# Kernel optimization log

Measured on AMD Instinct MI355X. Metric: run time of the kernel, lower is better.

## Reference

```python
import jax, jax.numpy as jnp
import numpy as np

B = 4096        # batch_size
D = 256         # feature_dim
N = 9000000     # dataset size (state buffer length)
G = 100         # num_groups
ALPHA = 0.5     # alpha_weight
GAMMA = 0.8
RHO = 8.0
LAM = 1.0       # lambada
ETA_P = 0.01
EPS = 1e-14
CLIP = 5.0


def setup_inputs() -> dict:
    key = jax.random.key(0)
    k = jax.random.split(key, 6)
    zis = jax.random.normal(k[0], (B, D), jnp.float32)
    zjs = jax.random.normal(k[1], (B, D), jnp.float32)
    # per-sample learned temperatures, small positive values
    taus_I = 0.01 + 0.2 * jax.random.uniform(k[2], (N,), jnp.float32)
    taus_T = 0.01 + 0.2 * jax.random.uniform(k[3], (N,), jnp.float32)
    group_info_I = jax.random.randint(k[4], (N,), 0, G, dtype=jnp.int32)
    group_info_T = jax.random.randint(k[5], (N,), 0, G, dtype=jnp.int32)
    ids = jnp.arange(B, dtype=jnp.int32)  # unique sample indices
    zeros_N = jnp.zeros((N,), jnp.float32)
    return {
        "zis": zis, "zjs": zjs,
        "s_I": zeros_N, "s_T": zeros_N, "b_I": zeros_N, "b_T": zeros_N,
        "z_I": jnp.zeros((G,), jnp.float32), "z_T": jnp.zeros((G,), jnp.float32),
        "p_I": jnp.ones((G,), jnp.float32) / G, "p_T": jnp.ones((G,), jnp.float32) / G,
        "taus_I": taus_I, "taus_T": taus_T,
        "ids": ids, "group_info_I": group_info_I, "group_info_T": group_info_T,
    }


def _l2norm(x):
    return x / jnp.maximum(jnp.linalg.norm(x, axis=1, keepdims=True), 1e-12)


def reference(zis, zjs, s_I, s_T, b_I, b_T, z_I, z_T, p_I, p_T,
              taus_I, taus_T, ids, group_info_I, group_info_T):
    zis = _l2norm(zis)
    zjs = _l2norm(zjs)
    sim = zis @ zjs.T                                   # [B, B]
    diag = jnp.diagonal(sim)                            # [B]
    mask_neg = 1.0 - jnp.eye(B, dtype=sim.dtype)
    image_diffs = sim - diag[:, None]
    text_diffs = sim - diag[None, :]

    tau_I = taus_I[ids]                                 # [B]
    tau_T = taus_T[ids]
    idt = jax.lax.stop_gradient(image_diffs / tau_I[:, None])
    tdt = jax.lax.stop_gradient(text_diffs / tau_T[None, :])

    # running max state (numerically-stable exp)
    old_b_I = b_I[ids]
    b_I_new = jnp.maximum(jnp.max(idt, axis=1), old_b_I)    # [B]
    old_b_T = b_T[ids]
    b_T_new = jnp.maximum(jnp.max(tdt, axis=0), old_b_T)    # [B]
    b_I = b_I.at[ids].set(b_I_new)
    b_T = b_T.at[ids].set(b_T_new)

    exp_I = jnp.exp(idt - b_I_new[:, None]) * mask_neg
    exp_T = jnp.exp(tdt - b_T_new[None, :]) * mask_neg
    g_I = jnp.sum(exp_I, axis=1)                         # [B]
    g_T = jnp.sum(exp_T, axis=0)                         # [B]

    # EMA of softmax denominators with max-rescaling
    s_I_new = (1.0 - GAMMA) * s_I[ids] * jnp.exp(old_b_I - b_I_new) + GAMMA * g_I
    s_T_new = (1.0 - GAMMA) * s_T[ids] * jnp.exp(old_b_T - b_T_new) + GAMMA * g_T
    s_I = s_I.at[ids].set(s_I_new)
    s_T = s_T.at[ids].set(s_T_new)
    s_I_c = jnp.maximum(s_I_new, EPS)
    s_T_c = jnp.maximum(s_T_new, EPS)

    w_I = exp_I / s_I_c[:, None]
    w_T = exp_T / s_T_c[None, :]

    gid_I = group_info_I[ids]                            # [B]
    gid_T = group_info_T[ids]
    gw_I = G * p_I[gid_I]                                # [B]
    gw_T = G * p_T[gid_T]

    image_loss = jnp.sum(w_I * gw_I[:, None] * image_diffs, axis=1)   # [B]
    text_loss = jnp.sum(w_T * gw_T[None, :] * text_diffs, axis=0)     # [B]
    total_loss = ALPHA * image_loss.mean() + (1.0 - ALPHA) * text_loss.mean()

    # per-group adversarial weight update
    F_I = tau_I * (jnp.log(s_I_c) + b_I_new + RHO)       # [B]
    F_T = tau_T * (jnp.log(s_T_c) + b_T_new + RHO)
    ones_b = jnp.ones((B,), sim.dtype)
    cnt_I = jnp.maximum(jax.ops.segment_sum(ones_b, gid_I, num_segments=G), 1.0)
    cnt_T = jnp.maximum(jax.ops.segment_sum(ones_b, gid_T, num_segments=G), 1.0)
    grad_p_I = jax.ops.segment_sum(F_I, gid_I, num_segments=G) / cnt_I
    grad_p_T = jax.ops.segment_sum(F_T, gid_T, num_segments=G) / cnt_T

    z_I = (1.0 - GAMMA) * z_I + GAMMA * grad_p_I
    z_T = (1.0 - GAMMA) * z_T + GAMMA * grad_p_T
    grad_hp_I = -LAM * jnp.log(p_I + EPS) - LAM
    grad_hp_T = -LAM * jnp.log(p_T + EPS) - LAM
    new_p_I = p_I * jnp.exp(2.0 * ETA_P * jnp.clip(z_I + grad_hp_I, -CLIP, CLIP))
    new_p_T = p_T * jnp.exp(2.0 * ETA_P * jnp.clip(z_T + grad_hp_T, -CLIP, CLIP))
    p_I = new_p_I / new_p_I.sum()
    p_T = new_p_T / new_p_T.sum()

    return total_loss, p_I, p_T
```

## Files before the change

kernel.cpp:

```cpp
#include <hip/hip_runtime.h>
#include <hip/hip_bf16.h>
#include <math.h>

#define BB 4096
#define DD 256
#define GG 100
#define GAMMA_C 0.8f
#define RHO_C 8.0f
#define ALPHA_C 0.5f
#define EPS_C 1e-14f
#define NSR 64
#define NSC 32

typedef __bf16 bf16x8 __attribute__((ext_vector_type(8)));
typedef float f32x16 __attribute__((ext_vector_type(16)));

__device__ inline int swzLoc(int r31, int k) {
    return ((k >> 4) << 9) | (((((k >> 3) & 1) << 5) | r31) << 3) | (k & 7);
}

__device__ inline float blockReduceSum(float v, float* lds) {
    for (int o = 32; o > 0; o >>= 1) v += __shfl_down(v, o);
    int lane = threadIdx.x & 63, wid = threadIdx.x >> 6;
    if (lane == 0) lds[wid] = v;
    __syncthreads();
    if (threadIdx.x == 0) {
        float r = lds[0];
        int nw = blockDim.x >> 6;
        for (int w = 1; w < nw; w++) r += lds[w];
        lds[0] = r;
    }
    __syncthreads();
    float r = lds[0];
    __syncthreads();
    return r;
}

__global__ void __launch_bounds__(256) norm_kernel(const float* __restrict__ zis,
                            const float* __restrict__ zjs,
                            ushort* __restrict__ zhi, ushort* __restrict__ zlo,
                            ushort* __restrict__ whi, ushort* __restrict__ wlo,
                            float* __restrict__ diag, float* __restrict__ acc) {
    __shared__ ushort st[4][8192];
    int rb = blockIdx.x;
    int wv = threadIdx.x >> 6, lane = threadIdx.x & 63;
    if (rb == 0) { acc[threadIdx.x] = 0.f; acc[threadIdx.x + 256] = 0.f; }
    for (int rr = 0; rr < 8; rr++) {
        int r = rb * 32 + wv * 8 + rr;
        float4 zv = *(const float4*)&zis[r * DD + lane * 4];
        float4 wv4 = *(const float4*)&zjs[r * DD + lane * 4];
        float sz = zv.x * zv.x + zv.y * zv.y + zv.z * zv.z + zv.w * zv.w;
        float sw = wv4.x * wv4.x + wv4.y * wv4.y + wv4.z * wv4.z + wv4.w * wv4.w;
        float dt = zv.x * wv4.x + zv.y * wv4.y + zv.z * wv4.z + zv.w * wv4.w;
        for (int mask = 1; mask <= 32; mask <<= 1) {
            sz += __shfl_xor(sz, mask);
            sw += __shfl_xor(sw, mask);
            dt += __shfl_xor(dt, mask);
        }
        float iz = 1.0f / fmaxf(sqrtf(sz), 1e-12f);
        float iw = 1.0f / fmaxf(sqrtf(sw), 1e-12f);
        if (lane == 0) diag[r] = dt * iz * iw;
        float nz[4] = {zv.x * iz, zv.y * iz, zv.z * iz, zv.w * iz};
        float nw[4] = {wv4.x * iw, wv4.y * iw, wv4.z * iw, wv4.w * iw};
        int r31 = wv * 8 + rr;
        for (int e = 0; e < 4; e++) {
            int k = lane * 4 + e;
            int li = swzLoc(r31, k);
            __hip_bfloat16 hz = __float2bfloat16(nz[e]);
            __hip_bfloat16 lz = __float2bfloat16(nz[e] - __bfloat162float(hz));
            __hip_bfloat16 hw = __float2bfloat16(nw[e]);
            __hip_bfloat16 lw = __float2bfloat16(nw[e] - __bfloat162float(hw));
            st[0][li] = *(ushort*)&hz;
            st[1][li] = *(ushort*)&lz;
            st[2][li] = *(ushort*)&hw;
            st[3][li] = *(ushort*)&lw;
        }
    }
    __syncthreads();
    size_t base = (size_t)rb * 8192;
    ushort* dsts[4] = {zhi + base, zlo + base, whi + base, wlo + base};
    for (int a = 0; a < 4; a++) {
        uint4* d = (uint4*)dsts[a];
        const uint4* s = (const uint4*)st[a];
        for (int it = 0; it < 4; it++) {
            int idx = it * 256 + threadIdx.x;
            d[idx] = s[idx];
        }
    }
}

__global__ void __launch_bounds__(256, 4) fused_tile(const ushort* __restrict__ Ahi,
        const ushort* __restrict__ Alo, const ushort* __restrict__ Bhi,
        const ushort* __restrict__ Blo, const float* __restrict__ diag,
        const float* __restrict__ tausI, const float* __restrict__ tausT,
        const int* __restrict__ ids,
        float* __restrict__ pmR, float* __restrict__ pgR, float* __restrict__ pwR,
        float* __restrict__ pmC, float* __restrict__ pgC, float* __restrict__ pwC) {
    __shared__ float rDiag[128], rITau[128];
    __shared__ float cDiag[64], cITau[64];
    __shared__ float cmS[4][64], cgS[4][64], cwS[4][64];

    int lane = threadIdx.x & 63;
    int wv = threadIdx.x >> 6;
    int bm = blockIdx.y * 128, bn = blockIdx.x * 64;
    int h = lane >> 5, cl = lane & 31;

    if (threadIdx.x < 128) {
        int r = bm + threadIdx.x;
        rDiag[threadIdx.x] = diag[r];
        rITau[threadIdx.x] = 1.0f / tausI[ids[r]];
    } else if (threadIdx.x < 192) {
        int c = bn + threadIdx.x - 128;
        cDiag[threadIdx.x - 128] = diag[c];
        cITau[threadIdx.x - 128] = 1.0f / tausT[ids[c]];
    }

    int aBase = (blockIdx.y * 4 + wv) * 8192;
    int b0 = (blockIdx.x * 2) * 8192;
    int b1 = b0 + 8192;
    int lofs = lane * 8;

    f32x16 acc[2] = {};
    f32x16 accT[2] = {};
#pragma unroll
    for (int s = 0; s < 16; s++) {
        int so = s * 512 + lofs;
        bf16x8 ah  = *(const bf16x8*)&Ahi[aBase + so];
        bf16x8 al  = *(const bf16x8*)&Alo[aBase + so];
        bf16x8 bh0 = *(const bf16x8*)&Bhi[b0 + so];
        bf16x8 bl0 = *(const bf16x8*)&Blo[b0 + so];
        bf16x8 bh1 = *(const bf16x8*)&Bhi[b1 + so];
        bf16x8 bl1 = *(const bf16x8*)&Blo[b1 + so];
        acc[0]  = __builtin_amdgcn_mfma_f32_32x32x16_bf16(ah, bh0, acc[0], 0, 0, 0);
        accT[0] = __builtin_amdgcn_mfma_f32_32x32x16_bf16(bh0, ah, accT[0], 0, 0, 0);
        acc[1]  = __builtin_amdgcn_mfma_f32_32x32x16_bf16(ah, bh1, acc[1], 0, 0, 0);
        accT[1] = __builtin_amdgcn_mfma_f32_32x32x16_bf16(bh1, ah, accT[1], 0, 0, 0);
        acc[0]  = __builtin_amdgcn_mfma_f32_32x32x16_bf16(ah, bl0, acc[0], 0, 0, 0);
        accT[0] = __builtin_amdgcn_mfma_f32_32x32x16_bf16(bh0, al, accT[0], 0, 0, 0);
        acc[1]  = __builtin_amdgcn_mfma_f32_32x32x16_bf16(ah, bl1, acc[1], 0, 0, 0);
        accT[1] = __builtin_amdgcn_mfma_f32_32x32x16_bf16(bh1, al, accT[1], 0, 0, 0);
        acc[0]  = __builtin_amdgcn_mfma_f32_32x32x16_bf16(al, bh0, acc[0], 0, 0, 0);
        accT[0] = __builtin_amdgcn_mfma_f32_32x32x16_bf16(bl0, ah, accT[0], 0, 0, 0);
        acc[1]  = __builtin_amdgcn_mfma_f32_32x32x16_bf16(al, bh1, acc[1], 0, 0, 0);
        accT[1] = __builtin_amdgcn_mfma_f32_32x32x16_bf16(bl1, ah, accT[1], 0, 0, 0);
    }
    __syncthreads();

    float cd2[2], cit2[2], cbloc[2], cg[2] = {}, cw[2] = {};
    for (int u = 0; u < 2; u++) {
        int clc = u * 32 + cl;
        cd2[u] = cDiag[clc];
        cit2[u] = cITau[clc];
        float m = -INFINITY;
        for (int reg = 0; reg < 16; reg++) m = fmaxf(m, acc[u][reg]);
        m = fmaxf(m, __shfl_xor(m, 32));
        cbloc[u] = (m - cd2[u]) * cit2[u];
    }
    for (int u = 0; u < 2; u++) {
        int gc = bn + u * 32 + cl;
        for (int reg = 0; reg < 16; reg++) {
            int gr = bm + wv * 32 + (reg & 3) + 4 * h + 8 * (reg >> 2);
            float v = acc[u][reg];
            bool off = gr != gc;
            float dvT = v - cd2[u];
            float eT = off ? __expf(dvT * cit2[u] - cbloc[u]) : 0.f;
            cg[u] += eT;
            cw[u] += eT * dvT;
        }
    }
    for (int u = 0; u < 2; u++) {
        cg[u] += __shfl_xor(cg[u], 32);
        cw[u] += __shfl_xor(cw[u], 32);
        if (h == 0) {
            cmS[wv][u * 32 + cl] = cbloc[u];
            cgS[wv][u * 32 + cl] = cg[u];
            cwS[wv][u * 32 + cl] = cw[u];
        }
    }
    __syncthreads();
    if (threadIdx.x < 64) {
        int c = threadIdx.x;
        float m = fmaxf(fmaxf(cmS[0][c], cmS[1][c]), fmaxf(cmS[2][c], cmS[3][c]));
        float g = 0.f, w = 0.f;
        for (int wq = 0; wq < 4; wq++) {
            float f = __expf(cmS[wq][c] - m);
            g += cgS[wq][c] * f;
            w += cwS[wq][c] * f;
        }
        size_t o = (size_t)blockIdx.y * BB + bn + c;
        pmC[o] = m;
        pgC[o] = g;
        pwC[o] = w;
    }

    {
        int gr = bm + wv * 32 + cl;
        float rd = rDiag[wv * 32 + cl];
        float rit = rITau[wv * 32 + cl];
        float m = -INFINITY;
        for (int u = 0; u < 2; u++)
            for (int reg = 0; reg < 16; reg++)
                m = fmaxf(m, accT[u][reg]);
        m = fmaxf(m, __shfl_xor(m, 32));
        float bloc = (m - rd) * rit;
        float rg = 0.f, rw = 0.f;
        for (int u = 0; u < 2; u++) {
            for (int reg = 0; reg < 16; reg++) {
                int gc = bn + u * 32 + (reg & 3) + 4 * h + 8 * (reg >> 2);
                float v = accT[u][reg];
                bool off = gr != gc;
                float dvI = v - rd;
                float eI = off ? __expf(dvI * rit - bloc) : 0.f;
                rg += eI;
                rw += eI * dvI;
            }
        }
        rg += __shfl_xor(rg, 32);
        rw += __shfl_xor(rw, 32);
        if (h == 0) {
            size_t o = (size_t)blockIdx.x * BB + bm + wv * 32 + cl;
            pmR[o] = bloc;
            pgR[o] = rg;
            pwR[o] = rw;
        }
    }
}

__global__ void __launch_bounds__(256) fin_kernel(
        const float* __restrict__ pmR, const float* __restrict__ pgR,
        const float* __restrict__ pwR, const float* __restrict__ pmC,
        const float* __restrict__ pgC, const float* __restrict__ pwC,
        const float* __restrict__ sI, const float* __restrict__ bI,
        const float* __restrict__ tausI, const int* __restrict__ gInfI,
        const float* __restrict__ pI,
        const float* __restrict__ sT, const float* __restrict__ bT,
        const float* __restrict__ tausT, const int* __restrict__ gInfT,
        const float* __restrict__ pT,
        const int* __restrict__ ids, float* __restrict__ acc,
        const float* __restrict__ zI, const float* __restrict__ zT,
        float* __restrict__ out) {
    __shared__ float lds[8];
    __shared__ float binF[GG], binC[GG];
    __shared__ float mS[4][64], gS[4][64], wS[4][64];
    __shared__ int lastFlag;
    if (threadIdx.x < GG) { binF[threadIdx.x] = 0.f; binC[threadIdx.x] = 0.f; }
    int side = blockIdx.x >> 6;
    int chunk = blockIdx.x & 63;
    int il = threadIdx.x & 63;
    int sg = threadIdx.x >> 6;
    int i = chunk * 64 + il;
    int ns = side ? NSC : NSR;
    const float* pm = side ? pmC : pmR;
    const float* pg = side ? pgC : pgR;
    const float* pw = side ? pwC : pwR;
    const float* sS = side ? sT : sI;
    const float* bS = side ? bT : bI;
    const float* taus = side ? tausT : tausI;
    const int* ginfo = side ? gInfT : gInfI;
    const float* pP = side ? pT : pI;

    float m = -INFINITY, g = 0.f, w = 0.f;
    for (int s = sg; s < ns; s += 4) {
        float pms = pm[(size_t)s * BB + i];
        float pgs = pg[(size_t)s * BB + i];
        float pws = pw[(size_t)s * BB + i];
        float mn = fmaxf(m, pms);
        float fo = __expf(m - mn);
        float fs = __expf(pms - mn);
        g = g * fo + pgs * fs;
        w = w * fo + pws * fs;
        m = mn;
    }
    mS[sg][il] = m;
    gS[sg][il] = g;
    wS[sg][il] = w;
    __syncthreads();

    float loss = 0.f;
    if (sg == 0) {
        int id = ids[i];
        float oldb = bS[id];
        float mm = fmaxf(fmaxf(mS[0][il], mS[1][il]), fmaxf(mS[2][il], mS[3][il]));
        float bfin = fmaxf(mm, oldb);
        float gg2 = 0.f, ww2 = 0.f;
        for (int q = 0; q < 4; q++) {
            float f = __expf(mS[q][il] - bfin);
            gg2 += gS[q][il] * f;
            ww2 += wS[q][il] * f;
        }
        float tau = taus[id];
        float snew = (1.f - GAMMA_C) * sS[id] * expf(oldb - bfin) + GAMMA_C * gg2;
        float sc = fmaxf(snew, EPS_C);
        int gid = ginfo[id];
        float gw = (float)GG * pP[gid];
        loss = gw * ww2 / sc;
        float F = tau * (logf(sc) + bfin + RHO_C);
        atomicAdd(&binF[gid], F);
        atomicAdd(&binC[gid], 1.0f);
    }
    float lsum = blockReduceSum(loss, lds);
    if (threadIdx.x == 0) atomicAdd(&acc[side], lsum);
    __syncthreads();
    if (threadIdx.x < GG) {
        atomicAdd(&acc[2 + side * 200 + threadIdx.x], binF[threadIdx.x]);
        atomicAdd(&acc[102 + side * 200 + threadIdx.x], binC[threadIdx.x]);
    }

    __threadfence();
    if (threadIdx.x == 0) {
        int old = atomicAdd((int*)&acc[408], 1);
        lastFlag = (old == 127);
    }
    __syncthreads();
    if (!lastFlag) return;

    int gg = threadIdx.x;
    float npI = 0.f, npT = 0.f;
    if (gg < GG) {
        float cI = __hip_atomic_load(&acc[102 + gg], __ATOMIC_RELAXED, __HIP_MEMORY_SCOPE_AGENT);
        float fI = __hip_atomic_load(&acc[2 + gg], __ATOMIC_RELAXED, __HIP_MEMORY_SCOPE_AGENT);
        float gpI = fI / fmaxf(cI, 1.f);
        float zi = (1.f - GAMMA_C) * zI[gg] + GAMMA_C * gpI;
        float ghpI = -logf(pI[gg] + EPS_C) - 1.f;
        float ti = fminf(fmaxf(zi + ghpI, -5.f), 5.f);
        npI = pI[gg] * expf(0.02f * ti);

        float cT = __hip_atomic_load(&acc[302 + gg], __ATOMIC_RELAXED, __HIP_MEMORY_SCOPE_AGENT);
        float fT = __hip_atomic_load(&acc[202 + gg], __ATOMIC_RELAXED, __HIP_MEMORY_SCOPE_AGENT);
        float gpT = fT / fmaxf(cT, 1.f);
        float zt = (1.f - GAMMA_C) * zT[gg] + GAMMA_C * gpT;
        float ghpT = -logf(pT[gg] + EPS_C) - 1.f;
        float tt = fminf(fmaxf(zt + ghpT, -5.f), 5.f);
        npT = pT[gg] * expf(0.02f * tt);
    }
    float sumI = blockReduceSum(npI, lds);
    float sumT = blockReduceSum(npT, lds);
    if (gg < GG) {
        out[1 + gg] = npI / sumI;
        out[101 + gg] = npT / sumT;
    }
    if (gg == 0) {
        float lI = __hip_atomic_load(&acc[0], __ATOMIC_RELAXED, __HIP_MEMORY_SCOPE_AGENT);
        float lT = __hip_atomic_load(&acc[1], __ATOMIC_RELAXED, __HIP_MEMORY_SCOPE_AGENT);
        out[0] = ALPHA_C * (lI / (float)BB) + (1.f - ALPHA_C) * (lT / (float)BB);
    }
}

extern "C" void kernel_launch(void* const* d_in, const int* in_sizes, int n_in,
                              void* d_out, int out_size, void* d_ws, size_t ws_size,
                              hipStream_t stream) {
    const float* zis   = (const float*)d_in[0];
    const float* zjs   = (const float*)d_in[1];
    const float* s_I   = (const float*)d_in[2];
    const float* s_T   = (const float*)d_in[3];
    const float* b_I   = (const float*)d_in[4];
    const float* b_T   = (const float*)d_in[5];
    const float* z_I   = (const float*)d_in[6];
    const float* z_T   = (const float*)d_in[7];
    const float* p_I   = (const float*)d_in[8];
    const float* p_T   = (const float*)d_in[9];
    const float* tausI = (const float*)d_in[10];
    const float* tausT = (const float*)d_in[11];
    const int*   ids   = (const int*)d_in[12];
    const int*   gInfI = (const int*)d_in[13];
    const int*   gInfT = (const int*)d_in[14];
    float* out = (float*)d_out;

    char* ws = (char*)d_ws;
    ushort* zhi = (ushort*)ws;
    ushort* zlo = zhi + (size_t)BB * DD;
    ushort* whi = zlo + (size_t)BB * DD;
    ushort* wlo = whi + (size_t)BB * DD;
    float* acc  = (float*)(wlo + (size_t)BB * DD);
    float* diag = acc + 512;
    float* pmR  = diag + BB;
    float* pgR  = pmR + (size_t)NSR * BB;
    float* pwR  = pgR + (size_t)NSR * BB;
    float* pmC  = pwR + (size_t)NSR * BB;
    float* pgC  = pmC + (size_t)NSC * BB;
    float* pwC  = pgC + (size_t)NSC * BB;

    norm_kernel<<<128, 256, 0, stream>>>(zis, zjs, zhi, zlo, whi, wlo, diag, acc);
    fused_tile<<<dim3(64, 32), 256, 0, stream>>>(zhi, zlo, whi, wlo, diag,
            tausI, tausT, ids, pmR, pgR, pwR, pmC, pgC, pwC);
    fin_kernel<<<128, 256, 0, stream>>>(pmR, pgR, pwR, pmC, pgC, pwC,
            s_I, b_I, tausI, gInfI, p_I, s_T, b_T, tausT, gInfT, p_T, ids, acc,
            z_I, z_T, out);
}
```

Measured before the change: 286.2 us.

## Replace transposed MFMA accumulation with LDS transpose of the sim tile

The fused tile kernel previously computed both sim and its transpose with a second set of MFMAs, doubling matrix-core work. It now computes only the sim tile and writes it to padded shared memory (stride 65), then reads rows back for the row-wise softmax-style reductions. This halves MFMA count and accumulator registers, at the cost of extra LDS traffic, a larger shared-memory footprint (about 33KB per block) that may lower occupancy, and slightly different summation order.

Result: faster. 270.2 us (-5.6%).

```diff
diff --git a/kernel.cpp b/kernel.cpp
--- a/kernel.cpp
+++ b/kernel.cpp
@@ -99,6 +99,7 @@
     __shared__ float rDiag[128], rITau[128];
     __shared__ float cDiag[64], cITau[64];
     __shared__ float cmS[4][64], cgS[4][64], cwS[4][64];
+    __shared__ float tr[4][32 * 65];
 
     int lane = threadIdx.x & 63;
     int wv = threadIdx.x >> 6;
@@ -121,7 +122,6 @@
     int lofs = lane * 8;
 
     f32x16 acc[2] = {};
-    f32x16 accT[2] = {};
 #pragma unroll
     for (int s = 0; s < 16; s++) {
         int so = s * 512 + lofs;
@@ -131,33 +131,31 @@
         bf16x8 bl0 = *(const bf16x8*)&Blo[b0 + so];
         bf16x8 bh1 = *(const bf16x8*)&Bhi[b1 + so];
         bf16x8 bl1 = *(const bf16x8*)&Blo[b1 + so];
-        acc[0]  = __builtin_amdgcn_mfma_f32_32x32x16_bf16(ah, bh0, acc[0], 0, 0, 0);
-        accT[0] = __builtin_amdgcn_mfma_f32_32x32x16_bf16(bh0, ah, accT[0], 0, 0, 0);
-        acc[1]  = __builtin_amdgcn_mfma_f32_32x32x16_bf16(ah, bh1, acc[1], 0, 0, 0);
-        accT[1] = __builtin_amdgcn_mfma_f32_32x32x16_bf16(bh1, ah, accT[1], 0, 0, 0);
-        acc[0]  = __builtin_amdgcn_mfma_f32_32x32x16_bf16(ah, bl0, acc[0], 0, 0, 0);
-        accT[0] = __builtin_amdgcn_mfma_f32_32x32x16_bf16(bh0, al, accT[0], 0, 0, 0);
-        acc[1]  = __builtin_amdgcn_mfma_f32_32x32x16_bf16(ah, bl1, acc[1], 0, 0, 0);
-        accT[1] = __builtin_amdgcn_mfma_f32_32x32x16_bf16(bh1, al, accT[1], 0, 0, 0);
-        acc[0]  = __builtin_amdgcn_mfma_f32_32x32x16_bf16(al, bh0, acc[0], 0, 0, 0);
-        accT[0] = __builtin_amdgcn_mfma_f32_32x32x16_bf16(bl0, ah, accT[0], 0, 0, 0);
-        acc[1]  = __builtin_amdgcn_mfma_f32_32x32x16_bf16(al, bh1, acc[1], 0, 0, 0);
-        accT[1] = __builtin_amdgcn_mfma_f32_32x32x16_bf16(bl1, ah, accT[1], 0, 0, 0);
-    }
-    __syncthreads();
-
+        acc[0] = __builtin_amdgcn_mfma_f32_32x32x16_bf16(ah, bh0, acc[0], 0, 0, 0);
+        acc[1] = __builtin_amdgcn_mfma_f32_32x32x16_bf16(ah, bh1, acc[1], 0, 0, 0);
+        acc[0] = __builtin_amdgcn_mfma_f32_32x32x16_bf16(ah, bl0, acc[0], 0, 0, 0);
+        acc[1] = __builtin_amdgcn_mfma_f32_32x32x16_bf16(ah, bl1, acc[1], 0, 0, 0);
+        acc[0] = __builtin_amdgcn_mfma_f32_32x32x16_bf16(al, bh0, acc[0], 0, 0, 0);
+        acc[1] = __builtin_amdgcn_mfma_f32_32x32x16_bf16(al, bh1, acc[1], 0, 0, 0);
+    }
+
+    __syncthreads();
     float cd2[2], cit2[2], cbloc[2], cg[2] = {}, cw[2] = {};
+#pragma unroll
     for (int u = 0; u < 2; u++) {
         int clc = u * 32 + cl;
         cd2[u] = cDiag[clc];
         cit2[u] = cITau[clc];
         float m = -INFINITY;
+#pragma unroll
         for (int reg = 0; reg < 16; reg++) m = fmaxf(m, acc[u][reg]);
         m = fmaxf(m, __shfl_xor(m, 32));
         cbloc[u] = (m - cd2[u]) * cit2[u];
     }
+#pragma unroll
     for (int u = 0; u < 2; u++) {
         int gc = bn + u * 32 + cl;
+#pragma unroll
         for (int reg = 0; reg < 16; reg++) {
             int gr = bm + wv * 32 + (reg & 3) + 4 * h + 8 * (reg >> 2);
             float v = acc[u][reg];
@@ -168,6 +166,7 @@
             cw[u] += eT * dvT;
         }
     }
+#pragma unroll
     for (int u = 0; u < 2; u++) {
         cg[u] += __shfl_xor(cg[u], 32);
         cw[u] += __shfl_xor(cw[u], 32);
@@ -177,7 +176,16 @@
             cwS[wv][u * 32 + cl] = cw[u];
         }
     }
-    __syncthreads();
+
+#pragma unroll
+    for (int u = 0; u < 2; u++)
+#pragma unroll
+        for (int reg = 0; reg < 16; reg++) {
+            int r = (reg & 3) + 4 * h + 8 * (reg >> 2);
+            tr[wv][r * 65 + u * 32 + cl] = acc[u][reg];
+        }
+    __syncthreads();
+
     if (threadIdx.x < 64) {
         int c = threadIdx.x;
         float m = fmaxf(fmaxf(cmS[0][c], cmS[1][c]), fmaxf(cmS[2][c], cmS[3][c]));
@@ -194,31 +202,31 @@
     }
 
     {
-        int gr = bm + wv * 32 + cl;
-        float rd = rDiag[wv * 32 + cl];
-        float rit = rITau[wv * 32 + cl];
+        int r = cl;
+        int grow = bm + wv * 32 + r;
+        float rd = rDiag[wv * 32 + r];
+        float rit = rITau[wv * 32 + r];
+        float vv[32];
+#pragma unroll
+        for (int j = 0; j < 32; j++) vv[j] = tr[wv][r * 65 + h * 32 + j];
         float m = -INFINITY;
-        for (int u = 0; u < 2; u++)
-            for (int reg = 0; reg < 16; reg++)
-                m = fmaxf(m, accT[u][reg]);
+#pragma unroll
+        for (int j = 0; j < 32; j++) m = fmaxf(m, vv[j]);
         m = fmaxf(m, __shfl_xor(m, 32));
         float bloc = (m - rd) * rit;
         float rg = 0.f, rw = 0.f;
-        for (int u = 0; u < 2; u++) {
-            for (int reg = 0; reg < 16; reg++) {
-                int gc = bn + u * 32 + (reg & 3) + 4 * h + 8 * (reg >> 2);
-                float v = accT[u][reg];
-                bool off = gr != gc;
-                float dvI = v - rd;
-                float eI = off ? __expf(dvI * rit - bloc) : 0.f;
-                rg += eI;
-                rw += eI * dvI;
-            }
+#pragma unroll
+        for (int j = 0; j < 32; j++) {
+            int gc = bn + h * 32 + j;
+            float dv = vv[j] - rd;
+            float e = (grow != gc) ? __expf(dv * rit - bloc) : 0.f;
+            rg += e;
+            rw += e * dv;
         }
         rg += __shfl_xor(rg, 32);
         rw += __shfl_xor(rw, 32);
         if (h == 0) {
-            size_t o = (size_t)blockIdx.x * BB + bm + wv * 32 + cl;
+            size_t o = (size_t)blockIdx.x * BB + grow;
             pmR[o] = bloc;
             pgR[o] = rg;
             pwR[o] = rw;
```
